# Kernel tuning notes

Hardware: AMD Instinct MI355X
Metric: run time of the kernel (lower is better)

Reference implementation:

```python
import jax, jax.numpy as jnp
import numpy as np

EPS = 1e-8
TEMPERATURE = 1.0


def setup_inputs() -> dict:
    key = jax.random.key(0)
    k1, k2, k3 = jax.random.split(key, 3)
    B, Q, K, H, D = 64, 64, 8192, 1, 64
    return {
        "query": jax.random.normal(k1, (B, Q, H, D), dtype=jnp.float32),
        "key": jax.random.normal(k2, (B, K, H, D), dtype=jnp.float32),
        "value": jax.random.normal(k3, (B, K, H, D), dtype=jnp.float32),
    }


def reference(query, key, value):
    # InvertedDotProductAttention(norm_type='mean', multi_head=False)
    d = query.shape[-1]
    q = query / jnp.sqrt(jnp.asarray(d, query.dtype))
    # logits: [B, H, Q, K]
    attn = jnp.einsum("bqhd,bkhd->bhqk", q, key)
    # inverted attention: softmax over the QUERY axis (-2)
    attn = jax.nn.softmax(attn / TEMPERATURE, axis=-2)
    attn = jnp.clip(attn, 0.0, 1.0)
    # renormalize over keys (norm_type == 'mean')
    attn = attn / (jnp.sum(attn, axis=-1, keepdims=True) + EPS)
    out = jnp.einsum("bhqk,bkhd->bqhd", attn, value)
    # single-head: squeeze heads dim
    out = jnp.squeeze(out, axis=-2)          # [B, Q, Dv]
    attn_weights = jnp.squeeze(attn, axis=-3)  # [B, Q, K]
    return out, attn_weights
```

## Files before the change

### kernel.cpp

```cpp
#include <hip/hip_runtime.h>
#include <cstddef>

#define NB 64
#define NQ 64
#define NK 8192
#define ND 64
#define KPB 256
#define NSLICE (NK / KPB)

typedef __attribute__((ext_vector_type(8))) short short8_t;
typedef __attribute__((ext_vector_type(4))) float float4_t;
typedef __attribute__((ext_vector_type(4))) unsigned short ushort4_t;

static __device__ __forceinline__ unsigned short f2bf(float f) {
    unsigned b = __float_as_uint(f);
    b += 0x7FFFu + ((b >> 16) & 1u);
    return (unsigned short)(b >> 16);
}
static __device__ __forceinline__ void split8(const float* f, short8_t& hi, short8_t& lo) {
#pragma unroll
    for (int j = 0; j < 8; ++j) {
        const unsigned u = __float_as_uint(f[j]);
        hi[j] = (short)(u >> 16);
        const float lof = f[j] - __uint_as_float(u & 0xFFFF0000u);
        lo[j] = (short)(__float_as_uint(lof) >> 16);
    }
}

__global__ __launch_bounds__(256, 3) void k_qk_rowsum(
    const float* __restrict__ query,
    const float* __restrict__ key,
    float* __restrict__ rowsum)
{
    __shared__ alignas(16) unsigned short Qhi[64 * 72];
    __shared__ alignas(16) unsigned short Qlo[64 * 72];

    const int tid  = threadIdx.x;
    const int b    = blockIdx.y;
    const int k0   = blockIdx.x * KPB;
    const int lane = tid & 63;
    const int w    = tid >> 6;
    const int lq   = lane & 15;
    const int lg   = lane >> 4;

    {
        const float* qb = query + (size_t)b * NQ * ND;
#pragma unroll
        for (int i = 0; i < 2; ++i) {
            const int o  = tid + 256 * i;
            const int q  = o >> 3;
            const int d0 = (o & 7) * 8;
            float f[8];
            *reinterpret_cast<float4*>(f)     = *reinterpret_cast<const float4*>(qb + q * ND + d0);
            *reinterpret_cast<float4*>(f + 4) = *reinterpret_cast<const float4*>(qb + q * ND + d0 + 4);
            short8_t h, l8;
            split8(f, h, l8);
            const int n    = q >> 4;
            const int l    = (q & 15) | (((d0 >> 3) & 3) << 4);
            const int dh   = d0 >> 5;
            const int base = l * 72 + n * 16 + dh * 8;
            *reinterpret_cast<short8_t*>(&Qhi[base]) = h;
            *reinterpret_cast<short8_t*>(&Qlo[base]) = l8;
        }
    }
    __syncthreads();

    short8_t bhi[4][2], blo[4][2];
#pragma unroll
    for (int n = 0; n < 4; ++n)
#pragma unroll
        for (int dh = 0; dh < 2; ++dh) {
            const int base = lane * 72 + n * 16 + dh * 8;
            bhi[n][dh] = *reinterpret_cast<const short8_t*>(&Qhi[base]);
            blo[n][dh] = *reinterpret_cast<const short8_t*>(&Qlo[base]);
        }

    float rsacc[4] = {0.f, 0.f, 0.f, 0.f};

#pragma unroll 1
    for (int s = 0; s < 4; ++s) {
        const int kbase = k0 + w * 64 + s * 16;
        const float* kr = key + ((size_t)b * NK + kbase + lq) * ND + lg * 8;
        short8_t ahi[2], alo[2];
#pragma unroll
        for (int dh = 0; dh < 2; ++dh) {
            float f[8];
            *reinterpret_cast<float4*>(f)     = *reinterpret_cast<const float4*>(kr + dh * 32);
            *reinterpret_cast<float4*>(f + 4) = *reinterpret_cast<const float4*>(kr + dh * 32 + 4);
            split8(f, ahi[dh], alo[dh]);
        }

        float4_t acc[4];
#pragma unroll
        for (int n = 0; n < 4; ++n) acc[n] = (float4_t){0.f, 0.f, 0.f, 0.f};
#pragma unroll
        for (int n = 0; n < 4; ++n)
#pragma unroll
            for (int dh = 0; dh < 2; ++dh) {
                acc[n] = __builtin_amdgcn_mfma_f32_16x16x32_bf16(ahi[dh], bhi[n][dh], acc[n], 0, 0, 0);
                acc[n] = __builtin_amdgcn_mfma_f32_16x16x32_bf16(ahi[dh], blo[n][dh], acc[n], 0, 0, 0);
                acc[n] = __builtin_amdgcn_mfma_f32_16x16x32_bf16(alo[dh], bhi[n][dh], acc[n], 0, 0, 0);
            }

        float m[4], z[4];
#pragma unroll
        for (int r = 0; r < 4; ++r) {
            m[r] = fmaxf(fmaxf(acc[0][r], acc[1][r]), fmaxf(acc[2][r], acc[3][r]));
            m[r] = fmaxf(m[r], __shfl_xor(m[r], 1, 64));
            m[r] = fmaxf(m[r], __shfl_xor(m[r], 2, 64));
            m[r] = fmaxf(m[r], __shfl_xor(m[r], 4, 64));
            m[r] = fmaxf(m[r], __shfl_xor(m[r], 8, 64));
            z[r] = 0.f;
        }
#pragma unroll
        for (int n = 0; n < 4; ++n)
#pragma unroll
            for (int r = 0; r < 4; ++r) {
                acc[n][r] = __expf((acc[n][r] - m[r]) * 0.125f);
                z[r] += acc[n][r];
            }
#pragma unroll
        for (int r = 0; r < 4; ++r) {
            z[r] += __shfl_xor(z[r], 1, 64);
            z[r] += __shfl_xor(z[r], 2, 64);
            z[r] += __shfl_xor(z[r], 4, 64);
            z[r] += __shfl_xor(z[r], 8, 64);
            z[r] = 1.f / z[r];
        }
#pragma unroll
        for (int n = 0; n < 4; ++n) {
            float rs = 0.f;
#pragma unroll
            for (int r = 0; r < 4; ++r) rs += acc[n][r] * z[r];
            rs += __shfl_xor(rs, 16, 64);
            rs += __shfl_xor(rs, 32, 64);
            rsacc[n] += rs;
        }
    }

    if (lg == 0) {
#pragma unroll
        for (int n = 0; n < 4; ++n)
            atomicAdd(&rowsum[b * NQ + lq + 16 * n], rsacc[n]);
    }
}

__global__ __launch_bounds__(256, 3) void k_attn_pv_mfma(
    const float* __restrict__ query,
    const float* __restrict__ key,
    const float* __restrict__ value,
    const float* __restrict__ rowsum,
    float* __restrict__ attn,
    float* __restrict__ partials)
{
    __shared__ alignas(16) unsigned short SH[64 * 264];
    __shared__ alignas(16) unsigned short Vhi[64 * 72];
    __shared__ alignas(16) unsigned short Vlo[64 * 72];
    __shared__ float rsL[64];

    const int tid  = threadIdx.x;
    const int b    = blockIdx.y;
    const int k0   = blockIdx.x * KPB;
    const int lane = tid & 63;
    const int w    = tid >> 6;
    const int lq   = lane & 15;
    const int lg   = lane >> 4;

    unsigned short* Qhi = SH;
    unsigned short* Qlo = SH + 64 * 72;

    const int vk4 = (tid >> 4) * 4;
    const int vd4 = (tid & 15) * 4;
    const float4* vg = reinterpret_cast<const float4*>(value + ((size_t)b * NK + k0) * ND);
    float vt[4][4];
#pragma unroll
    for (int r = 0; r < 4; ++r)
        *reinterpret_cast<float4*>(vt[r]) = vg[(vk4 + r) * 16 + (vd4 >> 2)];

    {
        const float* qb = query + (size_t)b * NQ * ND;
#pragma unroll
        for (int i = 0; i < 2; ++i) {
            const int o  = tid + 256 * i;
            const int q  = o >> 3;
            const int d0 = (o & 7) * 8;
            float f[8];
            *reinterpret_cast<float4*>(f)     = *reinterpret_cast<const float4*>(qb + q * ND + d0);
            *reinterpret_cast<float4*>(f + 4) = *reinterpret_cast<const float4*>(qb + q * ND + d0 + 4);
            short8_t h, l8;
            split8(f, h, l8);
            const int n    = q >> 4;
            const int l    = (q & 15) | (((d0 >> 3) & 3) << 4);
            const int dh   = d0 >> 5;
            const int base = l * 72 + n * 16 + dh * 8;
            *reinterpret_cast<short8_t*>(&Qhi[base]) = h;
            *reinterpret_cast<short8_t*>(&Qlo[base]) = l8;
        }
    }
    if (tid < 64) rsL[tid] = 1.f / (rowsum[b * NQ + tid] + 1e-8f);

    float kf[16];
    {
        const float* kr = key + ((size_t)b * NK + k0 + w * 64 + lq) * ND + lg * 8;
        *reinterpret_cast<float4*>(kf)      = *reinterpret_cast<const float4*>(kr);
        *reinterpret_cast<float4*>(kf + 4)  = *reinterpret_cast<const float4*>(kr + 4);
        *reinterpret_cast<float4*>(kf + 8)  = *reinterpret_cast<const float4*>(kr + 32);
        *reinterpret_cast<float4*>(kf + 12) = *reinterpret_cast<const float4*>(kr + 36);
    }
    __syncthreads();

    short8_t bhi[4][2], blo[4][2];
#pragma unroll
    for (int n = 0; n < 4; ++n)
#pragma unroll
        for (int dh = 0; dh < 2; ++dh) {
            const int base = lane * 72 + n * 16 + dh * 8;
            bhi[n][dh] = *reinterpret_cast<const short8_t*>(&Qhi[base]);
            blo[n][dh] = *reinterpret_cast<const short8_t*>(&Qlo[base]);
        }
    __syncthreads();

    unsigned short* pL = SH;
    float invr[4];
#pragma unroll
    for (int n = 0; n < 4; ++n) invr[n] = rsL[16 * n + lq];

#pragma unroll 1
    for (int s = 0; s < 4; ++s) {
        const int kbase = k0 + w * 64 + s * 16;

        short8_t ahi[2], alo[2];
        split8(kf, ahi[0], alo[0]);
        split8(kf + 8, ahi[1], alo[1]);

        if (s < 3) {
            const float* kr = key + ((size_t)b * NK + kbase + 16 + lq) * ND + lg * 8;
            *reinterpret_cast<float4*>(kf)      = *reinterpret_cast<const float4*>(kr);
            *reinterpret_cast<float4*>(kf + 4)  = *reinterpret_cast<const float4*>(kr + 4);
            *reinterpret_cast<float4*>(kf + 8)  = *reinterpret_cast<const float4*>(kr + 32);
            *reinterpret_cast<float4*>(kf + 12) = *reinterpret_cast<const float4*>(kr + 36);
        }

        float4_t acc[4];
#pragma unroll
        for (int n = 0; n < 4; ++n) acc[n] = (float4_t){0.f, 0.f, 0.f, 0.f};
#pragma unroll
        for (int n = 0; n < 4; ++n)
#pragma unroll
            for (int dh = 0; dh < 2; ++dh) {
                acc[n] = __builtin_amdgcn_mfma_f32_16x16x32_bf16(ahi[dh], bhi[n][dh], acc[n], 0, 0, 0);
                acc[n] = __builtin_amdgcn_mfma_f32_16x16x32_bf16(ahi[dh], blo[n][dh], acc[n], 0, 0, 0);
                acc[n] = __builtin_amdgcn_mfma_f32_16x16x32_bf16(alo[dh], bhi[n][dh], acc[n], 0, 0, 0);
            }

        float m[4], z[4];
#pragma unroll
        for (int r = 0; r < 4; ++r) {
            m[r] = fmaxf(fmaxf(acc[0][r], acc[1][r]), fmaxf(acc[2][r], acc[3][r]));
            m[r] = fmaxf(m[r], __shfl_xor(m[r], 1, 64));
            m[r] = fmaxf(m[r], __shfl_xor(m[r], 2, 64));
            m[r] = fmaxf(m[r], __shfl_xor(m[r], 4, 64));
            m[r] = fmaxf(m[r], __shfl_xor(m[r], 8, 64));
            z[r] = 0.f;
        }
#pragma unroll
        for (int n = 0; n < 4; ++n)
#pragma unroll
            for (int r = 0; r < 4; ++r) {
                acc[n][r] = __expf((acc[n][r] - m[r]) * 0.125f);
                z[r] += acc[n][r];
            }
#pragma unroll
        for (int r = 0; r < 4; ++r) {
            z[r] += __shfl_xor(z[r], 1, 64);
            z[r] += __shfl_xor(z[r], 2, 64);
            z[r] += __shfl_xor(z[r], 4, 64);
            z[r] += __shfl_xor(z[r], 8, 64);
            z[r] = 1.f / z[r];
        }

#pragma unroll
        for (int n = 0; n < 4; ++n) {
            float pf[4];
            ushort4_t u;
#pragma unroll
            for (int r = 0; r < 4; ++r) {
                pf[r] = acc[n][r] * z[r] * invr[n];
                u[r]  = f2bf(pf[r]);
            }
            *reinterpret_cast<float4*>(attn +
                ((size_t)(b * NQ + 16 * n + lq)) * NK + kbase + lg * 4) =
                *reinterpret_cast<float4*>(pf);
            *reinterpret_cast<ushort4_t*>(
                &pL[(16 * n + lq) * 264 + (kbase - k0) + lg * 4]) = u;
        }
    }

    float4_t oacc[4];
#pragma unroll
    for (int n = 0; n < 4; ++n) oacc[n] = (float4_t){0.f, 0.f, 0.f, 0.f};

#pragma unroll 1
    for (int c = 0; c < 4; ++c) {
        const int ms = (vk4 >> 3) & 3;
#pragma unroll
        for (int j = 0; j < 4; ++j) {
            ushort4_t h4, l4;
#pragma unroll
            for (int r = 0; r < 4; ++r) {
                const unsigned uu = __float_as_uint(vt[r][j]);
                h4[r] = (unsigned short)(uu >> 16);
                const float lof = vt[r][j] - __uint_as_float(uu & 0xFFFF0000u);
                l4[r] = (unsigned short)(__float_as_uint(lof) >> 16);
            }
            const int mrow = (vd4 + j) ^ ms;
            *reinterpret_cast<ushort4_t*>(&Vhi[mrow * 72 + vk4]) = h4;
            *reinterpret_cast<ushort4_t*>(&Vlo[mrow * 72 + vk4]) = l4;
        }
        if (c < 3) {
#pragma unroll
            for (int r = 0; r < 4; ++r)
                *reinterpret_cast<float4*>(vt[r]) =
                    vg[((c + 1) * 64 + vk4 + r) * 16 + (vd4 >> 2)];
        }
        __syncthreads();

#pragma unroll
        for (int h = 0; h < 2; ++h) {
            const int mrow = (16 * w + (lq ^ lg)) * 72;
            const short8_t vhi8 = *reinterpret_cast<const short8_t*>(&Vhi[mrow + h * 32 + lg * 8]);
            const short8_t vlo8 = *reinterpret_cast<const short8_t*>(&Vlo[mrow + h * 32 + lg * 8]);
#pragma unroll
            for (int n = 0; n < 4; ++n) {
                const short8_t pa = *reinterpret_cast<const short8_t*>(
                    &pL[(16 * n + lq) * 264 + c * 64 + h * 32 + lg * 8]);
                oacc[n] = __builtin_amdgcn_mfma_f32_16x16x32_bf16(pa, vhi8, oacc[n], 0, 0, 0);
                oacc[n] = __builtin_amdgcn_mfma_f32_16x16x32_bf16(pa, vlo8, oacc[n], 0, 0, 0);
            }
        }
        __syncthreads();
    }

    float* pb = partials + ((size_t)(b * NSLICE + blockIdx.x)) * (NQ * ND);
#pragma unroll
    for (int n = 0; n < 4; ++n)
#pragma unroll
        for (int r = 0; r < 4; ++r)
            pb[(16 * n + 4 * lg + r) * ND + 16 * w + lq] = oacc[n][r];
}

__global__ __launch_bounds__(256) void k_reduce_out(
    const float* __restrict__ partials,
    float* __restrict__ out)
{
    const int b   = blockIdx.y;
    const int idx = blockIdx.x * 256 + threadIdx.x;
    const float4* pb = reinterpret_cast<const float4*>(partials + (size_t)b * NSLICE * NQ * ND);
    float4 sum = make_float4(0.f, 0.f, 0.f, 0.f);
#pragma unroll
    for (int s = 0; s < NSLICE; ++s) {
        const float4 v = pb[(size_t)s * (NQ * ND / 4) + idx];
        sum.x += v.x; sum.y += v.y; sum.z += v.z; sum.w += v.w;
    }
    reinterpret_cast<float4*>(out + (size_t)b * NQ * ND)[idx] = sum;
}

extern "C" void kernel_launch(void* const* d_in, const int* in_sizes, int n_in,
                              void* d_out, int out_size, void* d_ws, size_t ws_size,
                              hipStream_t stream) {
    const float* query = (const float*)d_in[0];
    const float* key   = (const float*)d_in[1];
    const float* value = (const float*)d_in[2];

    float* out  = (float*)d_out;
    float* attn = (float*)d_out + (size_t)NB * NQ * ND;
    float* rowsum   = (float*)d_ws;
    float* partials = (float*)((char*)d_ws + 16384);

    hipMemsetAsync(rowsum, 0, (size_t)NB * NQ * sizeof(float), stream);

    dim3 g(NK / KPB, NB);
    k_qk_rowsum<<<g, 256, 0, stream>>>(query, key, rowsum);
    k_attn_pv_mfma<<<g, 256, 0, stream>>>(query, key, value, rowsum, attn, partials);
    k_reduce_out<<<dim3(4, NB), 256, 0, stream>>>(partials, out);
}
```

Measured before the change: 147.2 us.

## Prefetch key tiles, stage fp32 V in LDS, write attn from bf16 LDS copy

The QK rowsum kernel now double-buffers key loads in registers, fetching the next 16-row tile while the current one is split and multiplied. The PV kernel stages V as fp32 in a swizzled LDS tile and does the hi/lo bf16 split at read time, instead of splitting before the LDS write. The attention-weight output is no longer stored as fp32 inside the softmax loop. It is written at the end as coalesced full rows rebuilt from the bf16 copy kept in LDS. That last change lowers the precision of the returned attention weights to bf16, which risks tolerance failures and drops required fp32 output precision.

```diff
diff --git a/kernel.cpp b/kernel.cpp
--- a/kernel.cpp
+++ b/kernel.cpp
@@ -16,6 +16,9 @@
     unsigned b = __float_as_uint(f);
     b += 0x7FFFu + ((b >> 16) & 1u);
     return (unsigned short)(b >> 16);
+}
+static __device__ __forceinline__ float bf2f(unsigned short u) {
+    return __uint_as_float(((unsigned)u) << 16);
 }
 static __device__ __forceinline__ void split8(const float* f, short8_t& hi, short8_t& lo) {
 #pragma unroll
@@ -42,6 +45,15 @@
     const int w    = tid >> 6;
     const int lq   = lane & 15;
     const int lg   = lane >> 4;
+
+    float kf[16];
+    {
+        const float* kr = key + ((size_t)b * NK + k0 + w * 64 + lq) * ND + lg * 8;
+        *reinterpret_cast<float4*>(kf)      = *reinterpret_cast<const float4*>(kr);
+        *reinterpret_cast<float4*>(kf + 4)  = *reinterpret_cast<const float4*>(kr + 4);
+        *reinterpret_cast<float4*>(kf + 8)  = *reinterpret_cast<const float4*>(kr + 32);
+        *reinterpret_cast<float4*>(kf + 12) = *reinterpret_cast<const float4*>(kr + 36);
+    }
 
     {
         const float* qb = query + (size_t)b * NQ * ND;
@@ -80,14 +92,17 @@
 #pragma unroll 1
     for (int s = 0; s < 4; ++s) {
         const int kbase = k0 + w * 64 + s * 16;
-        const float* kr = key + ((size_t)b * NK + kbase + lq) * ND + lg * 8;
+
         short8_t ahi[2], alo[2];
-#pragma unroll
-        for (int dh = 0; dh < 2; ++dh) {
-            float f[8];
-            *reinterpret_cast<float4*>(f)     = *reinterpret_cast<const float4*>(kr + dh * 32);
-            *reinterpret_cast<float4*>(f + 4) = *reinterpret_cast<const float4*>(kr + dh * 32 + 4);
-            split8(f, ahi[dh], alo[dh]);
+        split8(kf, ahi[0], alo[0]);
+        split8(kf + 8, ahi[1], alo[1]);
+
+        if (s < 3) {
+            const float* kr = key + ((size_t)b * NK + kbase + 16 + lq) * ND + lg * 8;
+            *reinterpret_cast<float4*>(kf)      = *reinterpret_cast<const float4*>(kr);
+            *reinterpret_cast<float4*>(kf + 4)  = *reinterpret_cast<const float4*>(kr + 4);
+            *reinterpret_cast<float4*>(kf + 8)  = *reinterpret_cast<const float4*>(kr + 32);
+            *reinterpret_cast<float4*>(kf + 12) = *reinterpret_cast<const float4*>(kr + 36);
         }
 
         float4_t acc[4];
@@ -154,8 +169,7 @@
     float* __restrict__ partials)
 {
     __shared__ alignas(16) unsigned short SH[64 * 264];
-    __shared__ alignas(16) unsigned short Vhi[64 * 72];
-    __shared__ alignas(16) unsigned short Vlo[64 * 72];
+    __shared__ alignas(16) float Vs[64 * 68];
     __shared__ float rsL[64];
 
     const int tid  = threadIdx.x;
@@ -172,10 +186,19 @@
     const int vk4 = (tid >> 4) * 4;
     const int vd4 = (tid & 15) * 4;
     const float4* vg = reinterpret_cast<const float4*>(value + ((size_t)b * NK + k0) * ND);
-    float vt[4][4];
+    float4 vt[4];
 #pragma unroll
     for (int r = 0; r < 4; ++r)
-        *reinterpret_cast<float4*>(vt[r]) = vg[(vk4 + r) * 16 + (vd4 >> 2)];
+        vt[r] = vg[(vk4 + r) * 16 + (vd4 >> 2)];
+
+    float kf[16];
+    {
+        const float* kr = key + ((size_t)b * NK + k0 + w * 64 + lq) * ND + lg * 8;
+        *reinterpret_cast<float4*>(kf)      = *reinterpret_cast<const float4*>(kr);
+        *reinterpret_cast<float4*>(kf + 4)  = *reinterpret_cast<const float4*>(kr + 4);
+        *reinterpret_cast<float4*>(kf + 8)  = *reinterpret_cast<const float4*>(kr + 32);
+        *reinterpret_cast<float4*>(kf + 12) = *reinterpret_cast<const float4*>(kr + 36);
+    }
 
     {
         const float* qb = query + (size_t)b * NQ * ND;
@@ -198,15 +221,6 @@
         }
     }
     if (tid < 64) rsL[tid] = 1.f / (rowsum[b * NQ + tid] + 1e-8f);
-
-    float kf[16];
-    {
-        const float* kr = key + ((size_t)b * NK + k0 + w * 64 + lq) * ND + lg * 8;
-        *reinterpret_cast<float4*>(kf)      = *reinterpret_cast<const float4*>(kr);
-        *reinterpret_cast<float4*>(kf + 4)  = *reinterpret_cast<const float4*>(kr + 4);
-        *reinterpret_cast<float4*>(kf + 8)  = *reinterpret_cast<const float4*>(kr + 32);
-        *reinterpret_cast<float4*>(kf + 12) = *reinterpret_cast<const float4*>(kr + 36);
-    }
     __syncthreads();
 
     short8_t bhi[4][2], blo[4][2];
@@ -281,20 +295,15 @@
 
 #pragma unroll
         for (int n = 0; n < 4; ++n) {
-            float pf[4];
             ushort4_t u;
 #pragma unroll
-            for (int r = 0; r < 4; ++r) {
-                pf[r] = acc[n][r] * z[r] * invr[n];
-                u[r]  = f2bf(pf[r]);
-            }
-            *reinterpret_cast<float4*>(attn +
-                ((size_t)(b * NQ + 16 * n + lq)) * NK + kbase + lg * 4) =
-                *reinterpret_cast<float4*>(pf);
+            for (int r = 0; r < 4; ++r)
+                u[r] = f2bf(acc[n][r] * z[r] * invr[n]);
             *reinterpret_cast<ushort4_t*>(
                 &pL[(16 * n + lq) * 264 + (kbase - k0) + lg * 4]) = u;
         }
     }
+    __syncthreads();
 
     float4_t oacc[4];
 #pragma unroll
@@ -302,40 +311,34 @@
 
 #pragma unroll 1
     for (int c = 0; c < 4; ++c) {
-        const int ms = (vk4 >> 3) & 3;
-#pragma unroll
-        for (int j = 0; j < 4; ++j) {
-            ushort4_t h4, l4;
-#pragma unroll
-            for (int r = 0; r < 4; ++r) {
-                const unsigned uu = __float_as_uint(vt[r][j]);
-                h4[r] = (unsigned short)(uu >> 16);
-                const float lof = vt[r][j] - __uint_as_float(uu & 0xFFFF0000u);
-                l4[r] = (unsigned short)(__float_as_uint(lof) >> 16);
-            }
-            const int mrow = (vd4 + j) ^ ms;
-            *reinterpret_cast<ushort4_t*>(&Vhi[mrow * 72 + vk4]) = h4;
-            *reinterpret_cast<ushort4_t*>(&Vlo[mrow * 72 + vk4]) = l4;
+#pragma unroll
+        for (int r = 0; r < 4; ++r) {
+            const int row = vk4 + r;
+            const int xr  = ((row >> 3) & 3) << 3;
+            *reinterpret_cast<float4*>(&Vs[row * 68 + (vd4 ^ xr)]) = vt[r];
         }
         if (c < 3) {
 #pragma unroll
             for (int r = 0; r < 4; ++r)
-                *reinterpret_cast<float4*>(vt[r]) =
-                    vg[((c + 1) * 64 + vk4 + r) * 16 + (vd4 >> 2)];
+                vt[r] = vg[((c + 1) * 64 + vk4 + r) * 16 + (vd4 >> 2)];
         }
         __syncthreads();
 
 #pragma unroll
         for (int h = 0; h < 2; ++h) {
-            const int mrow = (16 * w + (lq ^ lg)) * 72;
-            const short8_t vhi8 = *reinterpret_cast<const short8_t*>(&Vhi[mrow + h * 32 + lg * 8]);
-            const short8_t vlo8 = *reinterpret_cast<const short8_t*>(&Vlo[mrow + h * 32 + lg * 8]);
+            float vf[8];
+            const int dsw = (16 * w + lq) ^ (lg << 3);
+#pragma unroll
+            for (int j = 0; j < 8; ++j)
+                vf[j] = Vs[(h * 32 + lg * 8 + j) * 68 + dsw];
+            short8_t vhi, vlo;
+            split8(vf, vhi, vlo);
 #pragma unroll
             for (int n = 0; n < 4; ++n) {
                 const short8_t pa = *reinterpret_cast<const short8_t*>(
                     &pL[(16 * n + lq) * 264 + c * 64 + h * 32 + lg * 8]);
-                oacc[n] = __builtin_amdgcn_mfma_f32_16x16x32_bf16(pa, vhi8, oacc[n], 0, 0, 0);
-                oacc[n] = __builtin_amdgcn_mfma_f32_16x16x32_bf16(pa, vlo8, oacc[n], 0, 0, 0);
+                oacc[n] = __builtin_amdgcn_mfma_f32_16x16x32_bf16(pa, vhi, oacc[n], 0, 0, 0);
+                oacc[n] = __builtin_amdgcn_mfma_f32_16x16x32_bf16(pa, vlo, oacc[n], 0, 0, 0);
             }
         }
         __syncthreads();
@@ -347,6 +350,21 @@
 #pragma unroll
         for (int r = 0; r < 4; ++r)
             pb[(16 * n + 4 * lg + r) * ND + 16 * w + lq] = oacc[n][r];
+
+    {
+        const int cl = tid & 63;
+#pragma unroll
+        for (int qq = 0; qq < 16; ++qq) {
+            const int row = qq * 4 + w;
+            const ushort4_t u = *reinterpret_cast<const ushort4_t*>(
+                &pL[row * 264 + cl * 4]);
+            float o[4];
+#pragma unroll
+            for (int e = 0; e < 4; ++e) o[e] = bf2f(u[e]);
+            *reinterpret_cast<float4*>(attn +
+                ((size_t)(b * NQ + row)) * NK + k0 + cl * 4) = *reinterpret_cast<float4*>(o);
+        }
+    }
 }
 
 __global__ __launch_bounds__(256) void k_reduce_out(
```

Measured after the change: 148.9 us. No clear change (+1.2%).

## Store unnormalized bf16 P in first pass, scale and do PV in second

Applied to the files above, without the earlier changes.

The first kernel now computes the query-axis softmax once, writes the probabilities as bf16 into a workspace buffer with a swizzled layout, and accumulates row sums from the rounded values. The second kernel no longer recomputes QK^T. It reads the stored P and V, scales by the inverse row sum, writes attn, and runs PV with single bf16 V instead of a hi/lo split. This removes the duplicate QK matmul and exp work at the cost of an extra 64MB bf16 round trip through memory and lower PV precision. It also adds an atomic fallback when the workspace is too small.

```diff
diff --git a/kernel.cpp b/kernel.cpp
--- a/kernel.cpp
+++ b/kernel.cpp
@@ -6,16 +6,21 @@
 #define NK 8192
 #define ND 64
 #define KPB 256
-#define NSLICE (NK / KPB)
+#define KSL 512
+#define NSLICE (NK / KSL)
 
 typedef __attribute__((ext_vector_type(8))) short short8_t;
+typedef __attribute__((ext_vector_type(8))) unsigned short ushort8_t;
+typedef __attribute__((ext_vector_type(4))) unsigned short ushort4_t;
 typedef __attribute__((ext_vector_type(4))) float float4_t;
-typedef __attribute__((ext_vector_type(4))) unsigned short ushort4_t;
 
 static __device__ __forceinline__ unsigned short f2bf(float f) {
     unsigned b = __float_as_uint(f);
     b += 0x7FFFu + ((b >> 16) & 1u);
     return (unsigned short)(b >> 16);
+}
+static __device__ __forceinline__ float bf2f(unsigned short u) {
+    return __uint_as_float(((unsigned)u) << 16);
 }
 static __device__ __forceinline__ void split8(const float* f, short8_t& hi, short8_t& lo) {
 #pragma unroll
@@ -27,13 +32,15 @@
     }
 }
 
-__global__ __launch_bounds__(256, 3) void k_qk_rowsum(
+__global__ __launch_bounds__(256, 3) void k_qk_p(
     const float* __restrict__ query,
     const float* __restrict__ key,
+    unsigned short* __restrict__ pstore,
     float* __restrict__ rowsum)
 {
-    __shared__ alignas(16) unsigned short Qhi[64 * 72];
-    __shared__ alignas(16) unsigned short Qlo[64 * 72];
+    __shared__ alignas(16) unsigned short SH[64 * 264];
+    unsigned short* Qhi = SH;
+    unsigned short* Qlo = SH + 64 * 72;
 
     const int tid  = threadIdx.x;
     const int b    = blockIdx.y;
@@ -42,6 +49,15 @@
     const int w    = tid >> 6;
     const int lq   = lane & 15;
     const int lg   = lane >> 4;
+
+    float kf[16];
+    {
+        const float* kr = key + ((size_t)b * NK + k0 + w * 64 + lq) * ND + lg * 8;
+        *reinterpret_cast<float4*>(kf)      = *reinterpret_cast<const float4*>(kr);
+        *reinterpret_cast<float4*>(kf + 4)  = *reinterpret_cast<const float4*>(kr + 4);
+        *reinterpret_cast<float4*>(kf + 8)  = *reinterpret_cast<const float4*>(kr + 32);
+        *reinterpret_cast<float4*>(kf + 12) = *reinterpret_cast<const float4*>(kr + 36);
+    }
 
     {
         const float* qb = query + (size_t)b * NQ * ND;
@@ -74,20 +90,25 @@
             bhi[n][dh] = *reinterpret_cast<const short8_t*>(&Qhi[base]);
             blo[n][dh] = *reinterpret_cast<const short8_t*>(&Qlo[base]);
         }
-
+    __syncthreads();
+
+    unsigned short* pL = SH;
     float rsacc[4] = {0.f, 0.f, 0.f, 0.f};
 
 #pragma unroll 1
     for (int s = 0; s < 4; ++s) {
         const int kbase = k0 + w * 64 + s * 16;
-        const float* kr = key + ((size_t)b * NK + kbase + lq) * ND + lg * 8;
+
         short8_t ahi[2], alo[2];
-#pragma unroll
-        for (int dh = 0; dh < 2; ++dh) {
-            float f[8];
-            *reinterpret_cast<float4*>(f)     = *reinterpret_cast<const float4*>(kr + dh * 32);
-            *reinterpret_cast<float4*>(f + 4) = *reinterpret_cast<const float4*>(kr + dh * 32 + 4);
-            split8(f, ahi[dh], alo[dh]);
+        split8(kf, ahi[0], alo[0]);
+        split8(kf + 8, ahi[1], alo[1]);
+
+        if (s < 3) {
+            const float* kr = key + ((size_t)b * NK + kbase + 16 + lq) * ND + lg * 8;
+            *reinterpret_cast<float4*>(kf)      = *reinterpret_cast<const float4*>(kr);
+            *reinterpret_cast<float4*>(kf + 4)  = *reinterpret_cast<const float4*>(kr + 4);
+            *reinterpret_cast<float4*>(kf + 8)  = *reinterpret_cast<const float4*>(kr + 32);
+            *reinterpret_cast<float4*>(kf + 12) = *reinterpret_cast<const float4*>(kr + 36);
         }
 
         float4_t acc[4];
@@ -127,11 +148,18 @@
             z[r] += __shfl_xor(z[r], 8, 64);
             z[r] = 1.f / z[r];
         }
+
 #pragma unroll
         for (int n = 0; n < 4; ++n) {
+            ushort4_t u;
             float rs = 0.f;
 #pragma unroll
-            for (int r = 0; r < 4; ++r) rs += acc[n][r] * z[r];
+            for (int r = 0; r < 4; ++r) {
+                u[r] = f2bf(acc[n][r] * z[r]);
+                rs += bf2f(u[r]);
+            }
+            *reinterpret_cast<ushort4_t*>(
+                &pL[(16 * n + lq) * 264 + w * 64 + s * 16 + lg * 4]) = u;
             rs += __shfl_xor(rs, 16, 64);
             rs += __shfl_xor(rs, 32, 64);
             rsacc[n] += rs;
@@ -143,210 +171,142 @@
         for (int n = 0; n < 4; ++n)
             atomicAdd(&rowsum[b * NQ + lq + 16 * n], rsacc[n]);
     }
-}
-
-__global__ __launch_bounds__(256, 3) void k_attn_pv_mfma(
-    const float* __restrict__ query,
-    const float* __restrict__ key,
+    __syncthreads();
+
+    {
+        const int cl = tid & 63;
+#pragma unroll
+        for (int t = 0; t < 16; ++t) {
+            const int row = t * 4 + w;
+            const ushort4_t u = *reinterpret_cast<const ushort4_t*>(&pL[row * 264 + cl * 4]);
+            const int c      = cl * 4;
+            const int half   = c >> 7;
+            const int slot   = (c & 127) >> 3;
+            const int sub    = (c >> 2) & 1;
+            const int sp     = slot ^ (row & 7);
+            *reinterpret_cast<ushort4_t*>(pstore +
+                ((size_t)(b * NQ + row)) * NK + k0 + half * 128 + sp * 8 + sub * 4) = u;
+        }
+    }
+}
+
+template<bool PART>
+__global__ __launch_bounds__(256, 4) void k_scale_pv(
+    const unsigned short* __restrict__ psrc,
     const float* __restrict__ value,
     const float* __restrict__ rowsum,
     float* __restrict__ attn,
-    float* __restrict__ partials)
+    float* __restrict__ dst)
 {
-    __shared__ alignas(16) unsigned short SH[64 * 264];
-    __shared__ alignas(16) unsigned short Vhi[64 * 72];
-    __shared__ alignas(16) unsigned short Vlo[64 * 72];
-    __shared__ float rsL[64];
+    __shared__ alignas(16) unsigned short pLu[64 * 128];
+    __shared__ alignas(16) unsigned short Vsu[128 * 68];
+    __shared__ float rsL[NQ];
 
     const int tid  = threadIdx.x;
     const int b    = blockIdx.y;
-    const int k0   = blockIdx.x * KPB;
+    const int ks   = blockIdx.x;
+    const int k0   = ks * KSL;
     const int lane = tid & 63;
     const int w    = tid >> 6;
     const int lq   = lane & 15;
     const int lg   = lane >> 4;
 
-    unsigned short* Qhi = SH;
-    unsigned short* Qlo = SH + 64 * 72;
-
-    const int vk4 = (tid >> 4) * 4;
-    const int vd4 = (tid & 15) * 4;
+    if (tid < NQ) rsL[tid] = 1.f / (rowsum[b * NQ + tid] + 1e-8f);
+
+    const unsigned short* pg = psrc + (size_t)b * NQ * NK;
     const float4* vg = reinterpret_cast<const float4*>(value + ((size_t)b * NK + k0) * ND);
-    float vt[4][4];
-#pragma unroll
-    for (int r = 0; r < 4; ++r)
-        *reinterpret_cast<float4*>(vt[r]) = vg[(vk4 + r) * 16 + (vd4 >> 2)];
-
-    {
-        const float* qb = query + (size_t)b * NQ * ND;
-#pragma unroll
-        for (int i = 0; i < 2; ++i) {
-            const int o  = tid + 256 * i;
-            const int q  = o >> 3;
-            const int d0 = (o & 7) * 8;
+
+    ushort8_t rp[4];
+    float4 rv[8];
+#pragma unroll
+    for (int i = 0; i < 4; ++i) {
+        const int idx = tid + 256 * i;
+        rp[i] = *reinterpret_cast<const ushort8_t*>(
+            &pg[(size_t)(idx >> 4) * NK + k0 + (idx & 15) * 8]);
+    }
+#pragma unroll
+    for (int i = 0; i < 8; ++i) rv[i] = vg[tid + 256 * i];
+
+    float4_t oacc[4];
+#pragma unroll
+    for (int n = 0; n < 4; ++n) oacc[n] = (float4_t){0.f, 0.f, 0.f, 0.f};
+
+#pragma unroll 1
+    for (int ht = 0; ht < 4; ++ht) {
+        __syncthreads();
+
+#pragma unroll
+        for (int i = 0; i < 4; ++i) {
+            const int idx  = tid + 256 * i;
+            const int row  = idx >> 4;
+            const int sl   = idx & 15;
+            const int slog = sl ^ (row & 7);
+            const float iv = rsL[row];
             float f[8];
-            *reinterpret_cast<float4*>(f)     = *reinterpret_cast<const float4*>(qb + q * ND + d0);
-            *reinterpret_cast<float4*>(f + 4) = *reinterpret_cast<const float4*>(qb + q * ND + d0 + 4);
-            short8_t h, l8;
-            split8(f, h, l8);
-            const int n    = q >> 4;
-            const int l    = (q & 15) | (((d0 >> 3) & 3) << 4);
-            const int dh   = d0 >> 5;
-            const int base = l * 72 + n * 16 + dh * 8;
-            *reinterpret_cast<short8_t*>(&Qhi[base]) = h;
-            *reinterpret_cast<short8_t*>(&Qlo[base]) = l8;
-        }
-    }
-    if (tid < 64) rsL[tid] = 1.f / (rowsum[b * NQ + tid] + 1e-8f);
-
-    float kf[16];
-    {
-        const float* kr = key + ((size_t)b * NK + k0 + w * 64 + lq) * ND + lg * 8;
-        *reinterpret_cast<float4*>(kf)      = *reinterpret_cast<const float4*>(kr);
-        *reinterpret_cast<float4*>(kf + 4)  = *reinterpret_cast<const float4*>(kr + 4);
-        *reinterpret_cast<float4*>(kf + 8)  = *reinterpret_cast<const float4*>(kr + 32);
-        *reinterpret_cast<float4*>(kf + 12) = *reinterpret_cast<const float4*>(kr + 36);
-    }
-    __syncthreads();
-
-    short8_t bhi[4][2], blo[4][2];
-#pragma unroll
-    for (int n = 0; n < 4; ++n)
-#pragma unroll
-        for (int dh = 0; dh < 2; ++dh) {
-            const int base = lane * 72 + n * 16 + dh * 8;
-            bhi[n][dh] = *reinterpret_cast<const short8_t*>(&Qhi[base]);
-            blo[n][dh] = *reinterpret_cast<const short8_t*>(&Qlo[base]);
-        }
-    __syncthreads();
-
-    unsigned short* pL = SH;
-    float invr[4];
-#pragma unroll
-    for (int n = 0; n < 4; ++n) invr[n] = rsL[16 * n + lq];
-
-#pragma unroll 1
-    for (int s = 0; s < 4; ++s) {
-        const int kbase = k0 + w * 64 + s * 16;
-
-        short8_t ahi[2], alo[2];
-        split8(kf, ahi[0], alo[0]);
-        split8(kf + 8, ahi[1], alo[1]);
-
-        if (s < 3) {
-            const float* kr = key + ((size_t)b * NK + kbase + 16 + lq) * ND + lg * 8;
-            *reinterpret_cast<float4*>(kf)      = *reinterpret_cast<const float4*>(kr);
-            *reinterpret_cast<float4*>(kf + 4)  = *reinterpret_cast<const float4*>(kr + 4);
-            *reinterpret_cast<float4*>(kf + 8)  = *reinterpret_cast<const float4*>(kr + 32);
-            *reinterpret_cast<float4*>(kf + 12) = *reinterpret_cast<const float4*>(kr + 36);
-        }
-
-        float4_t acc[4];
-#pragma unroll
-        for (int n = 0; n < 4; ++n) acc[n] = (float4_t){0.f, 0.f, 0.f, 0.f};
-#pragma unroll
-        for (int n = 0; n < 4; ++n)
-#pragma unroll
-            for (int dh = 0; dh < 2; ++dh) {
-                acc[n] = __builtin_amdgcn_mfma_f32_16x16x32_bf16(ahi[dh], bhi[n][dh], acc[n], 0, 0, 0);
-                acc[n] = __builtin_amdgcn_mfma_f32_16x16x32_bf16(ahi[dh], blo[n][dh], acc[n], 0, 0, 0);
-                acc[n] = __builtin_amdgcn_mfma_f32_16x16x32_bf16(alo[dh], bhi[n][dh], acc[n], 0, 0, 0);
-            }
-
-        float m[4], z[4];
-#pragma unroll
-        for (int r = 0; r < 4; ++r) {
-            m[r] = fmaxf(fmaxf(acc[0][r], acc[1][r]), fmaxf(acc[2][r], acc[3][r]));
-            m[r] = fmaxf(m[r], __shfl_xor(m[r], 1, 64));
-            m[r] = fmaxf(m[r], __shfl_xor(m[r], 2, 64));
-            m[r] = fmaxf(m[r], __shfl_xor(m[r], 4, 64));
-            m[r] = fmaxf(m[r], __shfl_xor(m[r], 8, 64));
-            z[r] = 0.f;
-        }
-#pragma unroll
-        for (int n = 0; n < 4; ++n)
-#pragma unroll
-            for (int r = 0; r < 4; ++r) {
-                acc[n][r] = __expf((acc[n][r] - m[r]) * 0.125f);
-                z[r] += acc[n][r];
-            }
-#pragma unroll
-        for (int r = 0; r < 4; ++r) {
-            z[r] += __shfl_xor(z[r], 1, 64);
-            z[r] += __shfl_xor(z[r], 2, 64);
-            z[r] += __shfl_xor(z[r], 4, 64);
-            z[r] += __shfl_xor(z[r], 8, 64);
-            z[r] = 1.f / z[r];
-        }
-
-#pragma unroll
-        for (int n = 0; n < 4; ++n) {
-            float pf[4];
-            ushort4_t u;
-#pragma unroll
-            for (int r = 0; r < 4; ++r) {
-                pf[r] = acc[n][r] * z[r] * invr[n];
-                u[r]  = f2bf(pf[r]);
-            }
-            *reinterpret_cast<float4*>(attn +
-                ((size_t)(b * NQ + 16 * n + lq)) * NK + kbase + lg * 4) =
-                *reinterpret_cast<float4*>(pf);
-            *reinterpret_cast<ushort4_t*>(
-                &pL[(16 * n + lq) * 264 + (kbase - k0) + lg * 4]) = u;
-        }
-    }
-
-    float4_t oacc[4];
-#pragma unroll
-    for (int n = 0; n < 4; ++n) oacc[n] = (float4_t){0.f, 0.f, 0.f, 0.f};
-
-#pragma unroll 1
-    for (int c = 0; c < 4; ++c) {
-        const int ms = (vk4 >> 3) & 3;
-#pragma unroll
-        for (int j = 0; j < 4; ++j) {
-            ushort4_t h4, l4;
-#pragma unroll
-            for (int r = 0; r < 4; ++r) {
-                const unsigned uu = __float_as_uint(vt[r][j]);
-                h4[r] = (unsigned short)(uu >> 16);
-                const float lof = vt[r][j] - __uint_as_float(uu & 0xFFFF0000u);
-                l4[r] = (unsigned short)(__float_as_uint(lof) >> 16);
-            }
-            const int mrow = (vd4 + j) ^ ms;
-            *reinterpret_cast<ushort4_t*>(&Vhi[mrow * 72 + vk4]) = h4;
-            *reinterpret_cast<ushort4_t*>(&Vlo[mrow * 72 + vk4]) = l4;
-        }
-        if (c < 3) {
-#pragma unroll
-            for (int r = 0; r < 4; ++r)
-                *reinterpret_cast<float4*>(vt[r]) =
-                    vg[((c + 1) * 64 + vk4 + r) * 16 + (vd4 >> 2)];
+            ushort8_t u;
+#pragma unroll
+            for (int j = 0; j < 8; ++j) {
+                f[j] = bf2f(rp[i][j]) * iv;
+                u[j] = f2bf(f[j]);
+            }
+            float* ap = attn + ((size_t)(b * NQ + row)) * NK + k0 + ht * 128 + slog * 8;
+            *reinterpret_cast<float4*>(ap)     = *reinterpret_cast<float4*>(f);
+            *reinterpret_cast<float4*>(ap + 4) = *reinterpret_cast<float4*>(f + 4);
+            *reinterpret_cast<ushort8_t*>(&pLu[idx * 8]) = u;
+        }
+#pragma unroll
+        for (int i = 0; i < 8; ++i) {
+            const int idx = tid + 256 * i;
+            ushort4_t v4;
+            v4[0] = f2bf(rv[i].x); v4[1] = f2bf(rv[i].y);
+            v4[2] = f2bf(rv[i].z); v4[3] = f2bf(rv[i].w);
+            *reinterpret_cast<ushort4_t*>(&Vsu[(idx >> 4) * 68 + (idx & 15) * 4]) = v4;
+        }
+
+        if (ht < 3) {
+            const int kn = k0 + (ht + 1) * 128;
+#pragma unroll
+            for (int i = 0; i < 4; ++i) {
+                const int idx = tid + 256 * i;
+                rp[i] = *reinterpret_cast<const ushort8_t*>(
+                    &pg[(size_t)(idx >> 4) * NK + kn + (idx & 15) * 8]);
+            }
+#pragma unroll
+            for (int i = 0; i < 8; ++i)
+                rv[i] = vg[(ht + 1) * 2048 + tid + 256 * i];
         }
         __syncthreads();
 
 #pragma unroll
-        for (int h = 0; h < 2; ++h) {
-            const int mrow = (16 * w + (lq ^ lg)) * 72;
-            const short8_t vhi8 = *reinterpret_cast<const short8_t*>(&Vhi[mrow + h * 32 + lg * 8]);
-            const short8_t vlo8 = *reinterpret_cast<const short8_t*>(&Vlo[mrow + h * 32 + lg * 8]);
+        for (int h = 0; h < 4; ++h) {
+            short8_t vb;
+#pragma unroll
+            for (int j = 0; j < 8; ++j)
+                vb[j] = (short)Vsu[(h * 32 + lg * 8 + j) * 68 + 16 * w + lq];
 #pragma unroll
             for (int n = 0; n < 4; ++n) {
                 const short8_t pa = *reinterpret_cast<const short8_t*>(
-                    &pL[(16 * n + lq) * 264 + c * 64 + h * 32 + lg * 8]);
-                oacc[n] = __builtin_amdgcn_mfma_f32_16x16x32_bf16(pa, vhi8, oacc[n], 0, 0, 0);
-                oacc[n] = __builtin_amdgcn_mfma_f32_16x16x32_bf16(pa, vlo8, oacc[n], 0, 0, 0);
-            }
-        }
-        __syncthreads();
-    }
-
-    float* pb = partials + ((size_t)(b * NSLICE + blockIdx.x)) * (NQ * ND);
-#pragma unroll
-    for (int n = 0; n < 4; ++n)
-#pragma unroll
-        for (int r = 0; r < 4; ++r)
-            pb[(16 * n + 4 * lg + r) * ND + 16 * w + lq] = oacc[n][r];
+                    &pLu[(16 * n + lq) * 128 + (((h * 4 + lg) ^ (lq & 7)) * 8)]);
+                oacc[n] = __builtin_amdgcn_mfma_f32_16x16x32_bf16(pa, vb, oacc[n], 0, 0, 0);
+            }
+        }
+    }
+
+    if (PART) {
+        float* pb = dst + ((size_t)(b * NSLICE + ks)) * (NQ * ND);
+#pragma unroll
+        for (int n = 0; n < 4; ++n)
+#pragma unroll
+            for (int r = 0; r < 4; ++r)
+                pb[(16 * n + 4 * lg + r) * ND + 16 * w + lq] = oacc[n][r];
+    } else {
+#pragma unroll
+        for (int n = 0; n < 4; ++n)
+#pragma unroll
+            for (int r = 0; r < 4; ++r)
+                atomicAdd(dst + ((size_t)(b * NQ + 16 * n + 4 * lg + r)) * ND + 16 * w + lq,
+                          oacc[n][r]);
+    }
 }
 
 __global__ __launch_bounds__(256) void k_reduce_out(
@@ -374,13 +334,27 @@
 
     float* out  = (float*)d_out;
     float* attn = (float*)d_out + (size_t)NB * NQ * ND;
-    float* rowsum   = (float*)d_ws;
-    float* partials = (float*)((char*)d_ws + 16384);
+
+    const size_t PB_BYTES   = (size_t)NB * NQ * NK * sizeof(unsigned short);
+    const size_t PART_BYTES = (size_t)NB * NSLICE * NQ * ND * sizeof(float);
+
+    float* rowsum = (float*)d_ws;
+    unsigned short* pbuf = (unsigned short*)((char*)d_ws + 16384);
+    float* partials = (float*)((char*)d_ws + 16384 + PB_BYTES);
+    const bool part = ws_size >= 16384 + PB_BYTES + PART_BYTES;
 
     hipMemsetAsync(rowsum, 0, (size_t)NB * NQ * sizeof(float), stream);
-
-    dim3 g(NK / KPB, NB);
-    k_qk_rowsum<<<g, 256, 0, stream>>>(query, key, rowsum);
-    k_attn_pv_mfma<<<g, 256, 0, stream>>>(query, key, value, rowsum, attn, partials);
-    k_reduce_out<<<dim3(4, NB), 256, 0, stream>>>(partials, out);
-}
+    if (!part)
+        hipMemsetAsync(out, 0, (size_t)NB * NQ * ND * sizeof(float), stream);
+
+    dim3 gA(NK / KPB, NB);
+    k_qk_p<<<gA, 256, 0, stream>>>(query, key, pbuf, rowsum);
+
+    dim3 gB(NK / KSL, NB);
+    if (part) {
+        k_scale_pv<true><<<gB, 256, 0, stream>>>(pbuf, value, rowsum, attn, partials);
+        k_reduce_out<<<dim3(4, NB), 256, 0, stream>>>(partials, out);
+    } else {
+        k_scale_pv<false><<<gB, 256, 0, stream>>>(pbuf, value, rowsum, attn, out);
+    }
+}
```

Result: faster. 119.3 us (-18.9%).
